# Kernel tuning notes

Measured on AMD Instinct MI355X. Metric: run time of the kernel, lower is better.

## Reference

```python
import jax, jax.numpy as jnp
import numpy as np
import math

D_MODEL = 1024
D_STATE = 64
D_CONV = 4
EXPAND = 2
D_INNER = EXPAND * D_MODEL
DT_RANK = max(16, D_MODEL // 16)
SEQ_LEN = 2048
BATCH = 4

def setup_inputs() -> dict:
    key = jax.random.key(0)
    ks = jax.random.split(key, 16)
    s = lambda *sh: 1.0 / math.sqrt(sh[-1])
    x = jax.random.normal(ks[0], (SEQ_LEN, BATCH, D_MODEL), jnp.float32)
    state = jnp.zeros((BATCH, D_INNER, D_STATE), jnp.float32)
    W_in = jax.random.normal(ks[1], (2 * D_INNER, D_MODEL), jnp.float32) * s(2 * D_INNER, D_MODEL)
    b_in = jnp.zeros((2 * D_INNER,), jnp.float32)
    conv_w = jax.random.normal(ks[2], (D_INNER, 1, D_CONV), jnp.float32) * s(1, D_CONV)
    conv_b = jnp.zeros((D_INNER,), jnp.float32)
    W_xp = jax.random.normal(ks[3], (DT_RANK + 2 * D_STATE, D_INNER), jnp.float32) * s(1, D_INNER)
    b_xp = jnp.zeros((DT_RANK + 2 * D_STATE,), jnp.float32)
    W_dt = jax.random.normal(ks[4], (D_INNER, DT_RANK), jnp.float32) * s(1, DT_RANK)
    # dt bias init as in module: softplus-inverse of dt in [1e-3, 0.1]
    dt = jnp.exp(jax.random.uniform(ks[5], (D_INNER,)) * (math.log(0.1) - math.log(0.001)) + math.log(0.001))
    b_dt = dt + jnp.log(-jnp.expm1(-dt))
    A_log = jnp.log(jnp.broadcast_to(jnp.arange(1, D_STATE + 1, dtype=jnp.float32)[None, :], (D_INNER, D_STATE)))
    D = jnp.ones((D_INNER,), jnp.float32)
    W_out = jax.random.normal(ks[6], (D_MODEL, D_INNER), jnp.float32) * s(1, D_INNER)
    b_out = jnp.zeros((D_MODEL,), jnp.float32)
    ln_g = jnp.ones((D_MODEL,), jnp.float32)
    ln_b = jnp.zeros((D_MODEL,), jnp.float32)
    return dict(x=x, state=state, W_in=W_in, b_in=b_in, conv_w=conv_w, conv_b=conv_b,
                W_xp=W_xp, b_xp=b_xp, W_dt=W_dt, b_dt=b_dt, A_log=A_log, D=D,
                W_out=W_out, b_out=b_out, ln_g=ln_g, ln_b=ln_b)

def _silu(v):
    return v * jax.nn.sigmoid(v)

def _forward(x, state, W_in, b_in, conv_w, conv_b, W_xp, b_xp, W_dt, b_dt, A_log, D, W_out, b_out, ln_g, ln_b):
    S, B, _ = x.shape
    xz = x @ W_in.T + b_in                      # [S,B,2*di]
    x_inner, z = jnp.split(xz, 2, axis=-1)      # [S,B,di] each
    # causal depthwise conv1d: pad left (d_conv-1), matching conv1d(pad=K-1)[..., :S]
    xc = jnp.transpose(x_inner, (1, 2, 0))      # [B,di,S]
    xc = jax.lax.conv_general_dilated(
        xc, conv_w, window_strides=(1,), padding=[(D_CONV - 1, 0)],
        dimension_numbers=('NCH', 'OIH', 'NCH'), feature_group_count=D_INNER)
    xc = xc + conv_b[None, :, None]
    x_conv = _silu(jnp.transpose(xc, (2, 0, 1)))  # [S,B,di]
    # input-dependent projections over full sequence
    xp = x_conv @ W_xp.T + b_xp                 # [S,B,dt_rank+2*ds]
    dt_low, B_seq, C_seq = jnp.split(xp, [DT_RANK, DT_RANK + D_STATE], axis=-1)
    # NOTE: original adds dt_proj.bias twice (Linear already includes it)
    dt = jax.nn.softplus(dt_low @ W_dt.T + 2.0 * b_dt)  # [S,B,di]
    A = -jnp.exp(A_log)                         # [di,ds]

    def step(carry, inp):
        dt_t, B_t, C_t, x_t = inp               # [B,di],[B,ds],[B,ds],[B,di]
        dA = jnp.exp(dt_t[..., None] * A)       # [B,di,ds]
        dBx = (dt_t * x_t)[..., None] * B_t[:, None, :]  # [B,di,ds]
        new = carry * dA + dBx
        y = jnp.einsum('bdn,bn->bd', new, C_t) + D * x_t
        return new, y

    final_state, ys = jax.lax.scan(step, state, (dt, B_seq, C_seq, x_conv))
    ys = ys * _silu(z)                          # [S,B,di]
    out = jnp.mean(ys, axis=0) @ W_out.T + b_out  # [B,d_model]
    mu = jnp.mean(out, axis=-1, keepdims=True)
    var = jnp.var(out, axis=-1, keepdims=True)
    out = (out - mu) / jnp.sqrt(var + 1e-5) * ln_g + ln_b
    return out, final_state

def reference(x, state, W_in, b_in, conv_w, conv_b, W_xp, b_xp, W_dt, b_dt, A_log, D, W_out, b_out, ln_g, ln_b):
    return _forward(x, state, W_in, b_in, conv_w, conv_b, W_xp, b_xp, W_dt, b_dt, A_log, D, W_out, b_out, ln_g, ln_b)
```

## Files before the change

kernel.cpp:

```cpp
#include <hip/hip_runtime.h>
#include <hip/hip_fp16.h>

typedef __attribute__((ext_vector_type(8))) short short8;
typedef __attribute__((ext_vector_type(8))) unsigned short u16x8;
typedef __attribute__((ext_vector_type(4))) float f32x4;

#define S_LEN 2048
#define BATCH 4
#define DM 1024
#define DI 2048
#define DS 64
#define DTR 64
#define XPW 192
#define NCH 8
#define CLEN 256

typedef const __attribute__((address_space(4))) unsigned* cu_as4;

__device__ __forceinline__ unsigned short f2bf(float f){
  unsigned u = __builtin_bit_cast(unsigned, f);
  u += 0x7fffu + ((u >> 16) & 1u);
  return (unsigned short)(u >> 16);
}
__device__ __forceinline__ float bf2f(unsigned short h){
  unsigned u = ((unsigned)h) << 16;
  return __builtin_bit_cast(float, u);
}
__device__ __forceinline__ void gload16(const void* g, void* l){
  __builtin_amdgcn_global_load_lds((const __attribute__((address_space(1))) void*)g,
                                   (__attribute__((address_space(3))) void*)l, 16, 0, 0);
}
__device__ __forceinline__ float siluf_(float v){ return v / (1.f + __expf(-v)); }

__global__ __launch_bounds__(256) void cvt_all_k(const float* __restrict__ i0, unsigned short* __restrict__ o0,
                                                 const float* __restrict__ i1, unsigned short* __restrict__ o1,
                                                 const float* __restrict__ i2, unsigned short* __restrict__ o2,
                                                 const float* __restrict__ i3, unsigned short* __restrict__ o3)
{
  int bid = blockIdx.x;
  const float* in; unsigned short* out; int base;
  if (bid < 8192)       { in = i0; out = o0; base = bid; }
  else if (bid < 12288) { in = i1; out = o1; base = bid - 8192; }
  else if (bid < 12672) { in = i2; out = o2; base = bid - 12288; }
  else                  { in = i3; out = o3; base = bid - 12672; }
  int i = (base * 256 + threadIdx.x) * 4;
  float4 v = *(const float4*)(in + i);
  ushort4 o;
  o.x = f2bf(v.x); o.y = f2bf(v.y); o.z = f2bf(v.z); o.w = f2bf(v.w);
  *(ushort4*)(out + i) = o;
}

template<int EPI>
__global__ __launch_bounds__(256)
void gemm_bt(const unsigned short* __restrict__ A, const unsigned short* __restrict__ B,
             const float* __restrict__ bias,
             int N, int K, int lda, int ldb,
             void* __restrict__ vp0, void* __restrict__ vp1,
             const void* __restrict__ vp2, const void* __restrict__ vp3, int nsilu)
{
  __shared__ unsigned short As[128 * 32];
  __shared__ unsigned short Bs[128 * 32];
  const int tid  = threadIdx.x;
  const int lane = tid & 63;
  const int wid  = tid >> 6;
  const int bm = blockIdx.x, bn = blockIdx.y;
  const int r0 = tid >> 2;
  const int c0 = (tid & 3) * 8;
  int brow0 = bn * 128 + r0;        if (brow0 > N - 1) brow0 = N - 1;
  int brow1 = bn * 128 + 64 + r0;   if (brow1 > N - 1) brow1 = N - 1;
  const unsigned short* pa0 = A + (size_t)(bm * 128 + r0) * lda + c0;
  const unsigned short* pa1 = A + (size_t)(bm * 128 + 64 + r0) * lda + c0;
  const unsigned short* pb0 = B + (size_t)brow0 * ldb + c0;
  const unsigned short* pb1 = B + (size_t)brow1 * ldb + c0;
  f32x4 acc[4][4] = {};
  const int fr = lane & 15, fq = lane >> 4;
  const int wm = (wid >> 1) * 64, wn = (wid & 1) * 64;
  const int aoff0 = (wm + fr) * 32 + fq * 8;
  const int boff0 = (wn + fr) * 32 + fq * 8;
  for (int k0 = 0; k0 < K; k0 += 32) {
    __syncthreads();
    gload16(pa0 + k0, &As[tid * 8]);
    gload16(pa1 + k0, &As[2048 + tid * 8]);
    gload16(pb0 + k0, &Bs[tid * 8]);
    gload16(pb1 + k0, &Bs[2048 + tid * 8]);
    __syncthreads();
    short8 av[4], bv[4];
#pragma unroll
    for (int i = 0; i < 4; i++) av[i] = *(const short8*)&As[aoff0 + i * 16 * 32];
#pragma unroll
    for (int i = 0; i < 4; i++) bv[i] = *(const short8*)&Bs[boff0 + i * 16 * 32];
#pragma unroll
    for (int i = 0; i < 4; i++)
#pragma unroll
      for (int j = 0; j < 4; j++)
        acc[i][j] = __builtin_amdgcn_mfma_f32_16x16x32_bf16(av[i], bv[j], acc[i][j], 0, 0, 0);
  }

  if constexpr (EPI == 0) {
    unsigned short* xpb = (unsigned short*)vp0;
    float* bcI = (float*)vp1;
#pragma unroll
    for (int i = 0; i < 4; i++) {
#pragma unroll
      for (int j = 0; j < 4; j++) {
        int gc = bn * 128 + wn + j * 16 + fr;
        if (gc >= N) continue;
        float bb = bias[gc];
#pragma unroll
        for (int e = 0; e < 4; e++) {
          int gr = bm * 128 + wm + i * 16 + fq * 4 + e;
          float v = acc[i][j][e] + bb;
          xpb[(size_t)gr * XPW + gc] = f2bf(v);
          if (gc >= 64 && gc < 128)      bcI[((size_t)gr * 64 + gc - 64) * 2 + 0] = v;
          else if (gc >= 128)            bcI[((size_t)gr * 64 + gc - 128) * 2 + 1] = v;
        }
      }
    }
  } else if constexpr (EPI == 2) {
    unsigned short* xib = (unsigned short*)vp0;
    unsigned short* grm = (unsigned short*)vp1;
#pragma unroll
    for (int i = 0; i < 4; i++) {
#pragma unroll
      for (int j = 0; j < 4; j++) {
        int gc = bn * 128 + wn + j * 16 + fr;
        float bb = bias[gc];
#pragma unroll
        for (int e = 0; e < 4; e++) {
          int gr = bm * 128 + wm + i * 16 + fq * 4 + e;
          float v = acc[i][j][e] + bb;
          if (gc < nsilu) xib[(size_t)gr * DI + gc] = f2bf(v);
          else            grm[(size_t)gr * DI + (gc - nsilu)] = f2bf(siluf_(v));
        }
      }
    }
  } else {
    unsigned* dtH = (unsigned*)vp0;
    unsigned* dxg = (unsigned*)vp1;
    const unsigned short* xcb = (const unsigned short*)vp2;
    const unsigned short* grm = (const unsigned short*)vp3;
#pragma unroll
    for (int j = 0; j < 4; j++) {
      int gc = bn * 128 + wn + j * 16 + fr;
      float bb2 = 2.f * bias[gc];
#pragma unroll
      for (int i = 0; i < 4; i++)
#pragma unroll
        for (int e = 0; e < 4; e++) {
          float v = acc[i][j][e] + bb2;
          acc[i][j][e] = fmaxf(v, 0.f) + log1pf(__expf(-fabsf(v)));
        }
    }
    __shared__ unsigned short hbuf[256 * 36];
    const int myc = wn >> 6;
    const int tbase = wm / 4;
    for (int cc = 0; cc < 2; ++cc) {
      __syncthreads();
      if (myc == cc) {
#pragma unroll
        for (int i = 0; i < 4; i++)
#pragma unroll
          for (int j = 0; j < 4; j++) {
            int dl = j * 16 + fr;
            int t_ = tbase + i * 4 + fq;
#pragma unroll
            for (int e = 0; e < 4; e++)
              hbuf[(e * 64 + dl) * 36 + t_] =
                __builtin_bit_cast(unsigned short, __float2half_rn(acc[i][j][e]));
          }
      }
      __syncthreads();
#pragma unroll
      for (int k = 0; k < 4; ++k) {
        int gidx = tid + k * 256;
        int t   = gidx & 31;
        int gl8 = (gidx >> 5) & 7;
        int e   = gidx >> 8;
        int R   = e * 64 + gl8 * 8;
        uint4 o;
        o.x = (unsigned)hbuf[(R+0)*36 + t] | ((unsigned)hbuf[(R+1)*36 + t] << 16);
        o.y = (unsigned)hbuf[(R+2)*36 + t] | ((unsigned)hbuf[(R+3)*36 + t] << 16);
        o.z = (unsigned)hbuf[(R+4)*36 + t] | ((unsigned)hbuf[(R+5)*36 + t] << 16);
        o.w = (unsigned)hbuf[(R+6)*36 + t] | ((unsigned)hbuf[(R+7)*36 + t] << 16);
        size_t G = (size_t)(bn * 16 + cc * 8 + gl8);
        *(uint4*)&dtH[(((size_t)e * 256 + G) * 2048 + bm * 32 + t) * 4] = o;
      }
#pragma unroll
      for (int k = 0; k < 4; ++k) {
        int gidx = tid + k * 256;
        int t   = gidx & 31;
        int gl8 = (gidx >> 5) & 7;
        int e   = gidx >> 8;
        int gr  = (bm * 32 + t) * 4 + e;
        int col = bn * 128 + cc * 64 + gl8 * 8;
        u16x8 xv = *(const u16x8*)&xcb[(size_t)gr * DI + col];
        u16x8 gv = *(const u16x8*)&grm[(size_t)gr * DI + col];
        int R = e * 64 + gl8 * 8;
        unsigned ow[8];
#pragma unroll
        for (int u = 0; u < 8; ++u) {
          float dt = __half2float(__builtin_bit_cast(__half, hbuf[(R + u) * 36 + t]));
          float dtx = dt * bf2f((unsigned short)xv[u]);
          ow[u] = ((unsigned)f2bf(dtx) << 16) | (unsigned)(unsigned short)gv[u];
        }
        size_t G = (size_t)(bn * 16 + cc * 8 + gl8);
        unsigned* dst = &dxg[(((size_t)e * 256 + G) * 2048 + bm * 32 + t) * 8];
        uint4 o0, o1;
        o0.x = ow[0]; o0.y = ow[1]; o0.z = ow[2]; o0.w = ow[3];
        o1.x = ow[4]; o1.y = ow[5]; o1.z = ow[6]; o1.w = ow[7];
        *(uint4*)dst = o0;
        *(uint4*)(dst + 4) = o1;
      }
    }
  }
}

__global__ __launch_bounds__(256) void convsxg_k(const unsigned short* __restrict__ xib,
                                                 const unsigned short* __restrict__ grm,
                                                 const float* __restrict__ cw,
                                                 const float* __restrict__ cb,
                                                 unsigned short* __restrict__ xcb,
                                                 float* __restrict__ sxg)
{
  const int d4 = blockIdx.x * 1024 + threadIdx.x * 4;
  const int b  = blockIdx.y;
  const int t0 = blockIdx.z * 16;
  float4 cwv[4]; float cbv[4];
#pragma unroll
  for (int j = 0; j < 4; ++j) { cwv[j] = *(const float4*)&cw[(d4 + j) * 4]; cbv[j] = cb[d4 + j]; }
  ushort4 z4; z4.x = z4.y = z4.z = z4.w = 0;
  ushort4 xm1 = (t0 >= 1) ? *(const ushort4*)&xib[((size_t)((t0 - 1) * 4 + b)) * DI + d4] : z4;
  ushort4 xm2 = (t0 >= 2) ? *(const ushort4*)&xib[((size_t)((t0 - 2) * 4 + b)) * DI + d4] : z4;
  ushort4 xm3 = (t0 >= 3) ? *(const ushort4*)&xib[((size_t)((t0 - 3) * 4 + b)) * DI + d4] : z4;
  float sa[4] = {0.f, 0.f, 0.f, 0.f};
  for (int tt = 0; tt < 16; ++tt) {
    const int t = t0 + tt;
    const size_t row = ((size_t)(t * 4 + b)) * DI + d4;
    ushort4 x0 = *(const ushort4*)&xib[row];
    ushort4 gv = *(const ushort4*)&grm[row];
    unsigned short xr[4] = {x0.x, x0.y, x0.z, x0.w};
    unsigned short r1[4] = {xm1.x, xm1.y, xm1.z, xm1.w};
    unsigned short r2[4] = {xm2.x, xm2.y, xm2.z, xm2.w};
    unsigned short r3[4] = {xm3.x, xm3.y, xm3.z, xm3.w};
    unsigned short gg[4] = {gv.x, gv.y, gv.z, gv.w};
    unsigned short ov[4];
#pragma unroll
    for (int j = 0; j < 4; ++j) {
      float s = cbv[j];
      s = fmaf(cwv[j].w, bf2f(xr[j]), s);
      s = fmaf(cwv[j].z, bf2f(r1[j]), s);
      s = fmaf(cwv[j].y, bf2f(r2[j]), s);
      s = fmaf(cwv[j].x, bf2f(r3[j]), s);
      ov[j] = f2bf(siluf_(s));
      sa[j] = fmaf(bf2f(ov[j]), bf2f(gg[j]), sa[j]);
    }
    ushort4 o; o.x = ov[0]; o.y = ov[1]; o.z = ov[2]; o.w = ov[3];
    *(ushort4*)&xcb[row] = o;
    xm3 = xm2; xm2 = xm1; xm1 = x0;
  }
#pragma unroll
  for (int j = 0; j < 4; ++j) atomicAdd(&sxg[b * DI + d4 + j], sa[j]);
}

__global__ __launch_bounds__(256) void scan_k(const unsigned* __restrict__ dtHg,
                                              const unsigned* __restrict__ dxgg,
                                              const float* __restrict__ bcI,
                                              const float* __restrict__ A_log,
                                              float* __restrict__ Pb,
                                              float* __restrict__ Eb,
                                              float* __restrict__ Fb,
                                              float* __restrict__ accp)
{
  const int tid  = threadIdx.x;
  const int lane = tid & 63;
  const int gw = __builtin_amdgcn_readfirstlane(blockIdx.x * 4 + (tid >> 6));
  const int b  = gw >> 11;
  const int c  = (gw >> 8) & 7;
  const int g  = gw & 255;
  const int d0 = g * 8;
  const float LOG2E = 1.4426950408889634f;
  float a2[8], st[8], Dr[8], Fr[8], acc[8];
#pragma unroll
  for (int j = 0; j < 8; ++j) {
    a2[j] = -__expf(A_log[(size_t)(d0 + j) * DS + lane]) * LOG2E;
    st[j] = 0.f; Dr[j] = 1.f; Fr[j] = 0.f; acc[j] = 0.f;
  }
  cu_as4 pdt = (cu_as4)(unsigned long long)(dtHg + (((size_t)(b * 256 + g)) * S_LEN + c * CLEN) * 4);
  cu_as4 pdx = (cu_as4)(unsigned long long)(dxgg + (((size_t)(b * 256 + g)) * S_LEN + c * CLEN) * 8);
  const float* pbc = bcI + (((size_t)(c * CLEN) * 4 + b) * 64 + lane) * 2;
#pragma unroll 2
  for (int t = 0; t < CLEN; ++t) {
    unsigned dw0 = pdt[t * 4 + 0], dw1 = pdt[t * 4 + 1];
    unsigned dw2 = pdt[t * 4 + 2], dw3 = pdt[t * 4 + 3];
    unsigned xs[8];
#pragma unroll
    for (int j = 0; j < 8; ++j) xs[j] = pdx[t * 8 + j];
    float2 bc = *(const float2*)(pbc + (size_t)t * 512);
    float dts[8];
    dts[0] = __half2float(__builtin_bit_cast(__half, (unsigned short)(dw0 & 0xffffu)));
    dts[1] = __half2float(__builtin_bit_cast(__half, (unsigned short)(dw0 >> 16)));
    dts[2] = __half2float(__builtin_bit_cast(__half, (unsigned short)(dw1 & 0xffffu)));
    dts[3] = __half2float(__builtin_bit_cast(__half, (unsigned short)(dw1 >> 16)));
    dts[4] = __half2float(__builtin_bit_cast(__half, (unsigned short)(dw2 & 0xffffu)));
    dts[5] = __half2float(__builtin_bit_cast(__half, (unsigned short)(dw2 >> 16)));
    dts[6] = __half2float(__builtin_bit_cast(__half, (unsigned short)(dw3 & 0xffffu)));
    dts[7] = __half2float(__builtin_bit_cast(__half, (unsigned short)(dw3 >> 16)));
#pragma unroll
    for (int j = 0; j < 8; ++j) {
      float dxs = __builtin_bit_cast(float, xs[j] & 0xffff0000u);
      float gsv = __builtin_bit_cast(float, xs[j] << 16);
      float dA = __builtin_amdgcn_exp2f(dts[j] * a2[j]);
      st[j] = fmaf(st[j], dA, dxs * bc.x);
      Dr[j] *= dA;
      float w = gsv * bc.y;
      acc[j] = fmaf(st[j], w, acc[j]);
      Fr[j] = fmaf(Dr[j], w, Fr[j]);
    }
  }
  const size_t sb = (((size_t)((b * NCH + c) * 256 + g)) * 8) * 64 + lane;
#pragma unroll
  for (int j = 0; j < 8; ++j) {
    Pb[sb + j * 64] = st[j];
    Eb[sb + j * 64] = Dr[j];
    Fb[sb + j * 64] = Fr[j];
  }
#pragma unroll
  for (int j = 0; j < 8; ++j)
#pragma unroll
    for (int m = 32; m; m >>= 1) acc[j] += __shfl_xor(acc[j], m, 64);
  if (lane == 0) {
#pragma unroll
    for (int j = 0; j < 8; ++j)
      accp[(b * NCH + c) * DI + d0 + j] = acc[j];
  }
}

__global__ __launch_bounds__(256) void fixup_k(const float* __restrict__ Pb,
                                               const float* __restrict__ Eb,
                                               const float* __restrict__ Fb,
                                               const float* __restrict__ accp,
                                               const float* __restrict__ state_in,
                                               float* __restrict__ accbuf,
                                               float* __restrict__ state_out)
{
  const int tid  = threadIdx.x;
  const int lane = tid & 63;
  const int gw = blockIdx.x * 4 + (tid >> 6);
  const int b  = gw >> 8;
  const int g  = gw & 255;
  const int d0 = g * 8;
  float S[8], v[8];
#pragma unroll
  for (int j = 0; j < 8; ++j) {
    S[j] = state_in[((size_t)(b * DI + d0 + j)) * DS + lane];
    v[j] = 0.f;
  }
#pragma unroll
  for (int c = 0; c < NCH; ++c) {
    const size_t sb = (((size_t)((b * NCH + c) * 256 + g)) * 8) * 64 + lane;
#pragma unroll
    for (int j = 0; j < 8; ++j) {
      float P = Pb[sb + j * 64], E = Eb[sb + j * 64], F = Fb[sb + j * 64];
      v[j] = fmaf(F, S[j], v[j]);
      S[j] = fmaf(E, S[j], P);
    }
  }
#pragma unroll
  for (int j = 0; j < 8; ++j)
    state_out[((size_t)(b * DI + d0 + j)) * DS + lane] = S[j];
#pragma unroll
  for (int j = 0; j < 8; ++j)
#pragma unroll
    for (int m = 32; m; m >>= 1) v[j] += __shfl_xor(v[j], m, 64);
  if (lane == 0) {
#pragma unroll
    for (int j = 0; j < 8; ++j) {
      float s = v[j];
#pragma unroll
      for (int c = 0; c < NCH; ++c) s += accp[(b * NCH + c) * DI + d0 + j];
      accbuf[b * DI + d0 + j] = s;
    }
  }
}

__global__ __launch_bounds__(256) void out_gemm_k(const float* __restrict__ accb,
                                                  const float* __restrict__ sxg,
                                                  const float* __restrict__ Dv,
                                                  const float* __restrict__ W_out,
                                                  const float* __restrict__ b_out,
                                                  float* __restrict__ outpre)
{
  int b = blockIdx.y;
  int m = blockIdx.x * 8 + (threadIdx.x >> 5);
  int dl = threadIdx.x & 31;
  const float* wr = W_out + (size_t)m * DI;
  const float* ac = accb + b * DI;
  const float* sx = sxg + b * DI;
  float p = 0.f;
  for (int dd = dl; dd < DI; dd += 32) {
    float av = fmaf(Dv[dd], sx[dd], ac[dd]);
    p = fmaf(wr[dd], av, p);
  }
#pragma unroll
  for (int s = 16; s; s >>= 1) p += __shfl_xor(p, s, 32);
  if (dl == 0) outpre[b * DM + m] = p * (1.f / 2048.f) + b_out[m];
}

__global__ __launch_bounds__(256) void ln_k(const float* __restrict__ outpre,
                                            const float* __restrict__ g,
                                            const float* __restrict__ bta,
                                            float* __restrict__ dout)
{
  int b = blockIdx.x;
  const float* row = outpre + b * DM;
  float s = 0.f, s2 = 0.f, vv[4];
#pragma unroll
  for (int i = 0; i < 4; i++) {
    float v = row[threadIdx.x + i * 256];
    vv[i] = v; s += v; s2 += v * v;
  }
#pragma unroll
  for (int m = 32; m; m >>= 1) { s += __shfl_xor(s, m, 64); s2 += __shfl_xor(s2, m, 64); }
  __shared__ float rs[4], rs2[4];
  int w = threadIdx.x >> 6;
  if ((threadIdx.x & 63) == 0) { rs[w] = s; rs2[w] = s2; }
  __syncthreads();
  float S = rs[0] + rs[1] + rs[2] + rs[3];
  float S2 = rs2[0] + rs2[1] + rs2[2] + rs2[3];
  float mu = S * (1.f / 1024.f);
  float var = S2 * (1.f / 1024.f) - mu * mu;
  float inv = rsqrtf(var + 1e-5f);
#pragma unroll
  for (int i = 0; i < 4; i++) {
    int c = threadIdx.x + i * 256;
    dout[b * DM + c] = (vv[i] - mu) * inv * g[c] + bta[c];
  }
}

extern "C" void kernel_launch(void* const* d_in, const int* in_sizes, int n_in,
                              void* d_out, int out_size, void* d_ws, size_t ws_size,
                              hipStream_t stream)
{
  const float* x      = (const float*)d_in[0];
  const float* state0 = (const float*)d_in[1];
  const float* W_in   = (const float*)d_in[2];
  const float* b_in   = (const float*)d_in[3];
  const float* conv_w = (const float*)d_in[4];
  const float* conv_b = (const float*)d_in[5];
  const float* W_xp   = (const float*)d_in[6];
  const float* b_xp   = (const float*)d_in[7];
  const float* W_dt   = (const float*)d_in[8];
  const float* b_dt   = (const float*)d_in[9];
  const float* A_log  = (const float*)d_in[10];
  const float* Dvec   = (const float*)d_in[11];
  const float* W_out  = (const float*)d_in[12];
  const float* b_out  = (const float*)d_in[13];
  const float* ln_g   = (const float*)d_in[14];
  const float* ln_b   = (const float*)d_in[15];
  float* out = (float*)d_out;

  const size_t MB = 1024 * 1024;
  char* ws = (char*)d_ws;
  unsigned short* grm  = (unsigned short*)(ws + 0);
  unsigned short* xcb  = (unsigned short*)(ws + 32  * MB);
  unsigned short* xib  = (unsigned short*)(ws + 64  * MB);
  unsigned*       dtH  = (unsigned*)(ws + 64  * MB);
  unsigned short* xb   = (unsigned short*)(ws + 96  * MB);
  unsigned short* wbin = (unsigned short*)(ws + 112 * MB);
  unsigned*       dxg  = (unsigned*)(ws + 96  * MB);
  unsigned short* xpb  = (unsigned short*)(ws + 160 * MB);
  float*          bcI  = (float*)(ws + 163 * MB);
  unsigned short* wbxp = (unsigned short*)(ws + 167 * MB);
  unsigned short* wbdt = (unsigned short*)(ws + 167 * MB + 786432);
  float*          sxg    = (float*)(ws + 168 * MB);
  float*          accb   = (float*)(ws + 168 * MB + 32768);
  float*          outpre = (float*)(ws + 168 * MB + 65536);
  float*          Pb   = (float*)(ws + 0);
  float*          Eb   = (float*)(ws + 16 * MB);
  float*          Fb   = (float*)(ws + 32 * MB);
  float*          accp = (float*)(ws + 48 * MB);

  cvt_all_k<<<12800, 256, 0, stream>>>(x, xb, W_in, wbin, W_xp, wbxp, W_dt, wbdt);
  hipMemsetAsync(sxg, 0, 4 * DI * sizeof(float), stream);
  gemm_bt<2><<<dim3(64, 32), 256, 0, stream>>>(xb, wbin, b_in, 4096, 1024, 1024, 1024,
                                               xib, grm, nullptr, nullptr, 2048);
  convsxg_k<<<dim3(2, 4, 128), 256, 0, stream>>>(xib, grm, conv_w, conv_b, xcb, sxg);
  gemm_bt<0><<<dim3(64, 2), 256, 0, stream>>>(xcb, wbxp, b_xp, 192, 2048, 2048, 2048,
                                              xpb, bcI, nullptr, nullptr, 0);
  gemm_bt<1><<<dim3(64, 16), 256, 0, stream>>>(xpb, wbdt, b_dt, 2048, 64, XPW, 64,
                                               dtH, dxg, xcb, grm, 0);
  scan_k<<<2048, 256, 0, stream>>>(dtH, dxg, bcI, A_log, Pb, Eb, Fb, accp);
  fixup_k<<<256, 256, 0, stream>>>(Pb, Eb, Fb, accp, state0, accb, out + 4096);
  out_gemm_k<<<dim3(128, 4), 256, 0, stream>>>(accb, sxg, Dvec, W_out, b_out, outpre);
  ln_k<<<4, 256, 0, stream>>>(outpre, ln_g, ln_b, out);
}
```

Measured before the change: 517.4 us.

## Split-K the x_proj GEMM with a reduction kernel and swizzle in_proj blocks

The x_proj GEMM launched only 128 blocks over a long K of 2048. It now splits K four ways, writes fp32 partial sums to a workspace buffer, and adds a small kernel that sums the partials, adds the bias and emits the bf16 and B/C outputs. The in_proj GEMM also remaps its block indices so neighbouring blocks share input tiles in cache. The cost is an extra kernel launch plus about 32 MB of partial-sum writes and reads.

Result: faster. 505.5 us (-2.3%).

```diff
diff --git a/kernel.cpp b/kernel.cpp
--- a/kernel.cpp
+++ b/kernel.cpp
@@ -63,7 +63,16 @@
   const int tid  = threadIdx.x;
   const int lane = tid & 63;
   const int wid  = tid >> 6;
-  const int bm = blockIdx.x, bn = blockIdx.y;
+  int bm, bn;
+  if constexpr (EPI == 2) {
+    int flat = blockIdx.y * 64 + blockIdx.x;
+    int swz = (flat & 7) * 256 + (flat >> 3);
+    bm = swz & 63; bn = swz >> 6;
+  } else {
+    bm = blockIdx.x; bn = blockIdx.y;
+  }
+  int k_lo = 0, k_hi = K;
+  if constexpr (EPI == 3) { k_lo = blockIdx.z * 512; k_hi = k_lo + 512; }
   const int r0 = tid >> 2;
   const int c0 = (tid & 3) * 8;
   int brow0 = bn * 128 + r0;        if (brow0 > N - 1) brow0 = N - 1;
@@ -77,7 +86,7 @@
   const int wm = (wid >> 1) * 64, wn = (wid & 1) * 64;
   const int aoff0 = (wm + fr) * 32 + fq * 8;
   const int boff0 = (wn + fr) * 32 + fq * 8;
-  for (int k0 = 0; k0 < K; k0 += 32) {
+  for (int k0 = k_lo; k0 < k_hi; k0 += 32) {
     __syncthreads();
     gload16(pa0 + k0, &As[tid * 8]);
     gload16(pa1 + k0, &As[2048 + tid * 8]);
@@ -96,23 +105,18 @@
         acc[i][j] = __builtin_amdgcn_mfma_f32_16x16x32_bf16(av[i], bv[j], acc[i][j], 0, 0, 0);
   }
 
-  if constexpr (EPI == 0) {
-    unsigned short* xpb = (unsigned short*)vp0;
-    float* bcI = (float*)vp1;
+  if constexpr (EPI == 3) {
+    float* xpp = (float*)vp0;
+    const size_t kb = (size_t)blockIdx.z * 8192 * 256;
 #pragma unroll
     for (int i = 0; i < 4; i++) {
 #pragma unroll
       for (int j = 0; j < 4; j++) {
         int gc = bn * 128 + wn + j * 16 + fr;
-        if (gc >= N) continue;
-        float bb = bias[gc];
 #pragma unroll
         for (int e = 0; e < 4; e++) {
           int gr = bm * 128 + wm + i * 16 + fq * 4 + e;
-          float v = acc[i][j][e] + bb;
-          xpb[(size_t)gr * XPW + gc] = f2bf(v);
-          if (gc >= 64 && gc < 128)      bcI[((size_t)gr * 64 + gc - 64) * 2 + 0] = v;
-          else if (gc >= 128)            bcI[((size_t)gr * 64 + gc - 128) * 2 + 1] = v;
+          xpp[kb + (size_t)gr * 256 + gc] = acc[i][j][e];
         }
       }
     }
@@ -213,6 +217,20 @@
       }
     }
   }
+}
+
+__global__ __launch_bounds__(192) void xpred_k(const float* __restrict__ xpp,
+                                               const float* __restrict__ bias,
+                                               unsigned short* __restrict__ xpb,
+                                               float* __restrict__ bcI)
+{
+  const int gr = blockIdx.x;
+  const int gc = threadIdx.x;
+  const size_t o = (size_t)gr * 256 + gc;
+  float v = xpp[o] + xpp[o + 2097152] + xpp[o + 2 * 2097152] + xpp[o + 3 * 2097152] + bias[gc];
+  xpb[(size_t)gr * XPW + gc] = f2bf(v);
+  if (gc >= 64 && gc < 128)      bcI[((size_t)gr * 64 + gc - 64) * 2 + 0] = v;
+  else if (gc >= 128)            bcI[((size_t)gr * 64 + gc - 128) * 2 + 1] = v;
 }
 
 __global__ __launch_bounds__(256) void convsxg_k(const unsigned short* __restrict__ xib,
@@ -467,6 +485,7 @@
   unsigned*       dtH  = (unsigned*)(ws + 64  * MB);
   unsigned short* xb   = (unsigned short*)(ws + 96  * MB);
   unsigned short* wbin = (unsigned short*)(ws + 112 * MB);
+  float*          xpp  = (float*)(ws + 96 * MB);
   unsigned*       dxg  = (unsigned*)(ws + 96  * MB);
   unsigned short* xpb  = (unsigned short*)(ws + 160 * MB);
   float*          bcI  = (float*)(ws + 163 * MB);
@@ -485,8 +504,9 @@
   gemm_bt<2><<<dim3(64, 32), 256, 0, stream>>>(xb, wbin, b_in, 4096, 1024, 1024, 1024,
                                                xib, grm, nullptr, nullptr, 2048);
   convsxg_k<<<dim3(2, 4, 128), 256, 0, stream>>>(xib, grm, conv_w, conv_b, xcb, sxg);
-  gemm_bt<0><<<dim3(64, 2), 256, 0, stream>>>(xcb, wbxp, b_xp, 192, 2048, 2048, 2048,
-                                              xpb, bcI, nullptr, nullptr, 0);
+  gemm_bt<3><<<dim3(64, 2, 4), 256, 0, stream>>>(xcb, wbxp, nullptr, 192, 2048, 2048, 2048,
+                                                 xpp, nullptr, nullptr, nullptr, 0);
+  xpred_k<<<8192, 192, 0, stream>>>(xpp, b_xp, xpb, bcI);
   gemm_bt<1><<<dim3(64, 16), 256, 0, stream>>>(xpb, wbdt, b_dt, 2048, 64, XPW, 64,
                                                dtH, dxg, xcb, grm, 0);
   scan_k<<<2048, 256, 0, stream>>>(dtH, dxg, bcI, A_log, Pb, Eb, Fb, accp);
```
